# Performance work log

Measured on AMD Instinct MI355X. Metric: run time of the kernel, lower is better.

## Reference

```python
import jax, jax.numpy as jnp
import numpy as np


def setup_inputs() -> dict:
    B, S, DK, DV, H = 2, 2048, 1024, 1024, 16
    ks = jax.random.split(jax.random.key(0), 7)
    keys = jax.random.normal(ks[0], (B, S, DK), jnp.float32)
    queries = jax.random.normal(ks[1], (B, S, DK), jnp.float32)
    values = jax.random.normal(ks[2], (B, S, DV), jnp.float32)
    # per-head projection weights, stored as [H, in, out] (torch Linear uses W.T; math-equivalent)
    WQ = jax.random.normal(ks[3], (H, DK, DK // H), jnp.float32) / np.sqrt(DK).astype(np.float32)
    WK = jax.random.normal(ks[4], (H, DK, DK // H), jnp.float32) / np.sqrt(DK).astype(np.float32)
    WV = jax.random.normal(ks[5], (H, DV, DV // H), jnp.float32) / np.sqrt(DV).astype(np.float32)
    WO = jax.random.normal(ks[6], (DV, DV), jnp.float32) / np.sqrt(DV).astype(np.float32)
    return {"keys": keys, "queries": queries, "values": values,
            "WQ": WQ, "WK": WK, "WV": WV, "WO": WO, "masking": 1}


def reference(keys, queries, values, WQ, WK, WV, WO, masking):
    B, Sq, _ = queries.shape
    Sk = keys.shape[1]
    # batched per-head projections (original loops over heads in Python)
    Q = jnp.einsum('bqd,hde->bhqe', queries, WQ)   # [B,H,Sq,dh]
    K = jnp.einsum('bkd,hde->bhke', keys, WK)      # [B,H,Sk,dh]
    V = jnp.einsum('bkd,hde->bhke', values, WV)    # [B,H,Sk,dvh]
    q_idx = jnp.arange(Sq)[:, None]
    k_idx = jnp.arange(Sk)[None, :]
    causal = k_idx <= q_idx
    # NOTE: original never applies the slope m; bias = (i - j) for i<=j else 0, same for all heads
    bias = jnp.where(causal, (k_idx - q_idx).astype(jnp.float32), 0.0)
    scale = np.float32(1.0 / np.sqrt(Sk))  # original divides by sqrt(keys.shape[1])
    y = (jnp.einsum('bhqe,bhke->bhqk', Q, K) + bias) * scale
    if masking:
        y = jnp.where(causal, y, -jnp.inf)
    # original: F.softmax(y, 1) on [B,Sq,Sk] -> softmax over the QUERY axis
    z = jax.nn.softmax(y, axis=2)
    out = jnp.einsum('bhqk,bhke->bhqe', z, V)      # [B,H,Sq,dvh]
    out = out.transpose(0, 2, 1, 3).reshape(B, Sq, -1)  # concat heads on last dim
    return out @ WO
```

## Files before the change

### kernel.cpp

```cpp
#include <hip/hip_runtime.h>
#include <math.h>

#define SEQ    2048
#define DMODEL 1024
#define NH     16
#define DH     64
#define NB     2
#define BHN    (NB*NH)

static constexpr float SCALE  = 0.02209708691207961f;
static constexpr float SCALE2 = 0.02209708691207961f * 1.4426950408889634f;

typedef __attribute__((ext_vector_type(8))) short short8;
typedef __attribute__((ext_vector_type(4))) short short4v;
typedef __attribute__((ext_vector_type(4))) float f32x4;

__device__ __forceinline__ short f2bf(float f) {
    union { float f; unsigned u; } v; v.f = f;
    unsigned r = (v.u + 0x7FFFu + ((v.u >> 16) & 1u)) >> 16;
    return (short)r;
}

__device__ __forceinline__ unsigned pack_bf2(float a, float b) {
    union { float f; unsigned u; } ua, ub; ua.f = a; ub.f = b;
    return __builtin_amdgcn_perm(ub.u + 0x8000u, ua.u + 0x8000u, 0x07060302u);
}

__device__ __forceinline__ float bf2f(short s) {
    union { unsigned u; float f; } v; v.u = ((unsigned)(unsigned short)s) << 16;
    return v.f;
}

__device__ __forceinline__ float exp2_fast(float x) {
    float r;
    __asm__("v_exp_f32 %0, %1" : "=v"(r) : "v"(x));
    return r;
}

__device__ __forceinline__ void load16_lds(const short* g, short* l) {
    __builtin_amdgcn_global_load_lds(
        (const __attribute__((address_space(1))) unsigned int*)g,
        (__attribute__((address_space(3))) unsigned int*)l,
        16, 0, 0);
}

__device__ __forceinline__ void stage_rows(const short* g, short* s, int t, int ldg, int nIter) {
    int wave = t >> 6, lane = t & 63;
    #pragma unroll
    for (int i = 0; i < 4; ++i) {
        if (i >= nIter) break;
        int E   = i * 2048 + wave * 512 + lane * 8;
        int row = E >> 6;
        int blk = (lane & 7) ^ (row & 7);
        load16_lds(g + (size_t)row * ldg + blk * 8, s + i * 2048 + wave * 512);
    }
}

__device__ __forceinline__ short8 frag_sw(const short* s, int rowbase, int ks, int lane) {
    int m   = rowbase + (lane & 15);
    int q   = lane >> 4;
    int blk = (ks * 4 + q) ^ (m & 7);
    return *(const short8*)(s + m * 64 + blk * 8);
}

__global__ __launch_bounds__(256) void convert_all(
    const float* __restrict__ q, const float* __restrict__ k, const float* __restrict__ v,
    short* __restrict__ Xq, short* __restrict__ Xk, short* __restrict__ Xv,
    const float* __restrict__ WQ, const float* __restrict__ WK,
    const float* __restrict__ WV, const float* __restrict__ WO,
    short* __restrict__ WQt, short* __restrict__ WKt,
    short* __restrict__ WVt, short* __restrict__ WOt)
{
    __shared__ float Ts[64][68];
    const int lin = blockIdx.x;
    const int t = threadIdx.x;

    if (lin < 6144) {
        const int z = lin / 2048, bx = lin - z * 2048;
        const float* src = (z == 0) ? q : (z == 1) ? k : v;
        short* dst = (z == 0) ? Xq : (z == 1) ? Xk : Xv;
        size_t idx = ((size_t)bx * 256 + t) * 8;
        float4 a = *(const float4*)(src + idx);
        float4 b = *(const float4*)(src + idx + 4);
        short8 o;
        o[0] = f2bf(a.x); o[1] = f2bf(a.y); o[2] = f2bf(a.z); o[3] = f2bf(a.w);
        o[4] = f2bf(b.x); o[5] = f2bf(b.y); o[6] = f2bf(b.z); o[7] = f2bf(b.w);
        *(short8*)(dst + idx) = o;
        return;
    }

    const int wl = lin - 6144;
    const int z = wl >> 8, rem = wl & 255;
    const int k0 = (rem & 15) * 64;
    const int ny = rem >> 4;
    const float* W = (z == 0) ? WQ : (z == 1) ? WK : (z == 2) ? WV : WO;
    short* Wt = (z == 0) ? WQt : (z == 1) ? WKt : (z == 2) ? WVt : WOt;

    const int tr = t >> 4, tc4 = (t & 15) * 4;
    #pragma unroll
    for (int i = 0; i < 4; ++i) {
        int row = tr + i * 16;
        float4 v4;
        if (z < 3) v4 = *(const float4*)(W + (size_t)ny * DMODEL * DH + (size_t)(k0 + row) * DH + tc4);
        else       v4 = *(const float4*)(W + (size_t)(k0 + row) * DMODEL + ny * 64 + tc4);
        Ts[tc4 + 0][row] = v4.x; Ts[tc4 + 1][row] = v4.y;
        Ts[tc4 + 2][row] = v4.z; Ts[tc4 + 3][row] = v4.w;
    }
    __syncthreads();
    #pragma unroll
    for (int i = 0; i < 4; ++i) {
        int nl = tr + i * 16;
        short4v o;
        o[0] = f2bf(Ts[nl][tc4 + 0]); o[1] = f2bf(Ts[nl][tc4 + 1]);
        o[2] = f2bf(Ts[nl][tc4 + 2]); o[3] = f2bf(Ts[nl][tc4 + 3]);
        *(short4v*)(Wt + (size_t)(ny * 64 + nl) * DMODEL + k0 + tc4) = o;
    }
}

__global__ __launch_bounds__(256) void gemm_nt(
    const short* __restrict__ A0, const short* __restrict__ A1, const short* __restrict__ A2,
    const short* __restrict__ B0, const short* __restrict__ B1, const short* __restrict__ B2,
    short* __restrict__ Y0, short* __restrict__ Y1, short* __restrict__ Y2)
{
    const int z = blockIdx.z;
    const short* X  = (z == 0) ? A0 : (z == 1) ? A1 : A2;
    const short* Wt = (z == 0) ? B0 : (z == 1) ? B1 : B2;
    short* Y        = (z == 0) ? Y0 : (z == 1) ? Y1 : Y2;
    const bool vOrient = (z == 2);

    const int lin = blockIdx.y * 8 + blockIdx.x;
    const int n0 = (lin >> 5) * 128;
    const int m0 = (lin & 31) * 128;

    __shared__ short As[128 * 64];
    __shared__ short Bs[128 * 64];

    const int t = threadIdx.x;
    const int wave = t >> 6, lane = t & 63;
    const int wrow = (wave >> 1) * 64, wcol = (wave & 1) * 64;
    const int quad = lane >> 4, l15 = lane & 15;

    f32x4 acc[4][4];
    #pragma unroll
    for (int i = 0; i < 4; ++i)
        #pragma unroll
        for (int j = 0; j < 4; ++j)
            acc[i][j] = (f32x4)0.f;

    for (int k0 = 0; k0 < DMODEL; k0 += 64) {
        __syncthreads();
        stage_rows(X  + (size_t)m0 * DMODEL + k0, As, t, DMODEL, 4);
        stage_rows(Wt + (size_t)n0 * DMODEL + k0, Bs, t, DMODEL, 4);
        __syncthreads();
        if (!vOrient) {
            #pragma unroll
            for (int ks = 0; ks < 2; ++ks) {
                short8 xf[4], wf[4];
                #pragma unroll
                for (int i = 0; i < 4; ++i) xf[i] = frag_sw(As, wrow + i * 16, ks, lane);
                #pragma unroll
                for (int i = 0; i < 4; ++i) wf[i] = frag_sw(Bs, wcol + i * 16, ks, lane);
                #pragma unroll
                for (int a = 0; a < 4; ++a)
                    #pragma unroll
                    for (int b = 0; b < 4; ++b)
                        acc[a][b] = __builtin_amdgcn_mfma_f32_16x16x32_bf16(
                            wf[a], xf[b], acc[a][b], 0, 0, 0);
            }
        } else {
            #pragma unroll
            for (int ks = 0; ks < 2; ++ks) {
                short8 xf[4], wf[4];
                #pragma unroll
                for (int i = 0; i < 4; ++i) xf[i] = frag_sw(As, wrow + i * 16, ks, lane);
                #pragma unroll
                for (int i = 0; i < 4; ++i) wf[i] = frag_sw(Bs, wcol + i * 16, ks, lane);
                #pragma unroll
                for (int a = 0; a < 4; ++a)
                    #pragma unroll
                    for (int b = 0; b < 4; ++b)
                        acc[a][b] = __builtin_amdgcn_mfma_f32_16x16x32_bf16(
                            xf[a], wf[b], acc[a][b], 0, 0, 0);
            }
        }
    }

    if (vOrient) {
        #pragma unroll
        for (int a = 0; a < 4; ++a) {
            #pragma unroll
            for (int b = 0; b < 4; ++b) {
                int m = m0 + wrow + a * 16 + quad * 4;
                int n = n0 + wcol + b * 16 + l15;
                int bb = m >> 11, s = m & 2047, h = n >> 6, e = n & 63;
                short4v o;
                #pragma unroll
                for (int i = 0; i < 4; ++i) o[i] = f2bf(acc[a][b][i]);
                *(short4v*)(Y + ((size_t)((bb * NH + h) * DH + e)) * SEQ + s) = o;
            }
        }
    } else {
        #pragma unroll
        for (int a = 0; a < 4; ++a) {
            #pragma unroll
            for (int b = 0; b < 4; ++b) {
                int n = n0 + wcol + a * 16 + quad * 4;
                int m = m0 + wrow + b * 16 + l15;
                int bb = m >> 11, s = m & 2047, h = n >> 6, e = n & 63;
                short4v o;
                #pragma unroll
                for (int i = 0; i < 4; ++i) o[i] = f2bf(acc[a][b][i]);
                *(short4v*)(Y + ((size_t)((bb * NH + h) * SEQ + s)) * DH + e) = o;
            }
        }
    }
}

__global__ __launch_bounds__(256) void gemm_out(
    const short* __restrict__ X, const short* __restrict__ Wt,
    float* __restrict__ outF)
{
    const int lin = blockIdx.x;
    const int m0 = (lin & 31) * 128;
    const int n0 = (lin >> 5) * 64;

    __shared__ short As[2][128 * 64];
    __shared__ short Bs[2][64 * 64];

    const int t = threadIdx.x;
    const int wave = t >> 6, lane = t & 63;
    const int wrow = (wave >> 1) * 64, wcol = (wave & 1) * 32;
    const int quad = lane >> 4, l15 = lane & 15;

    f32x4 acc[2][4];
    #pragma unroll
    for (int i = 0; i < 2; ++i)
        #pragma unroll
        for (int j = 0; j < 4; ++j)
            acc[i][j] = (f32x4)0.f;

    stage_rows(X  + (size_t)m0 * DMODEL, As[0], t, DMODEL, 4);
    stage_rows(Wt + (size_t)n0 * DMODEL, Bs[0], t, DMODEL, 2);
    __syncthreads();

    int cur = 0;
    for (int it = 0; it < 16; ++it) {
        if (it + 1 < 16) {
            const int k0 = (it + 1) * 64;
            stage_rows(X  + (size_t)m0 * DMODEL + k0, As[cur ^ 1], t, DMODEL, 4);
            stage_rows(Wt + (size_t)n0 * DMODEL + k0, Bs[cur ^ 1], t, DMODEL, 2);
        }
        #pragma unroll
        for (int ks = 0; ks < 2; ++ks) {
            short8 xf[4], wf[2];
            #pragma unroll
            for (int i = 0; i < 4; ++i) xf[i] = frag_sw(As[cur], wrow + i * 16, ks, lane);
            #pragma unroll
            for (int i = 0; i < 2; ++i) wf[i] = frag_sw(Bs[cur], wcol + i * 16, ks, lane);
            #pragma unroll
            for (int a = 0; a < 2; ++a)
                #pragma unroll
                for (int b = 0; b < 4; ++b)
                    acc[a][b] = __builtin_amdgcn_mfma_f32_16x16x32_bf16(
                        wf[a], xf[b], acc[a][b], 0, 0, 0);
        }
        __syncthreads();
        cur ^= 1;
    }

    #pragma unroll
    for (int a = 0; a < 2; ++a) {
        #pragma unroll
        for (int b = 0; b < 4; ++b) {
            int n = n0 + wcol + a * 16 + quad * 4;
            int m = m0 + wrow + b * 16 + l15;
            float4 o = make_float4(acc[a][b][0], acc[a][b][1], acc[a][b][2], acc[a][b][3]);
            *(float4*)(outF + (size_t)m * DMODEL + n) = o;
        }
    }
}

__global__ __launch_bounds__(256) void stats_mfma(
    const short* __restrict__ Qg, const short* __restrict__ Kg,
    short* __restrict__ Vt, const int* __restrict__ mask_p)
{
    const int gblk = blockIdx.x;
    const int masking = mask_p[0];

    __shared__ short Ks[64 * 64];
    __shared__ short Qs[2][128 * 64];
    __shared__ float rsh[64];

    const int t = threadIdx.x;
    const int wave = t >> 6, lane = t & 63;
    const int quad = lane >> 4, l15 = lane & 15;

    for (int item = 0; item < 2; ++item) {
        const int w  = item ? (1023 - gblk) : gblk;
        const int kt = w >> 5, bh = w & 31;
        const int k0 = kt * 64;

        const int qb0 = masking ? (kt >> 1) : 0;
        const int q0s = qb0 * 128;
        if (item) __syncthreads();
        stage_rows(Kg + ((size_t)bh * SEQ + k0) * DH, Ks, t, DH, 2);
        stage_rows(Qg + ((size_t)bh * SEQ + q0s) * DH, Qs[0], t, DH, 4);
        __syncthreads();

        short8 Kf[2];
        Kf[0] = frag_sw(Ks, wave * 16, 0, lane);
        Kf[1] = frag_sw(Ks, wave * 16, 1, lane);

        int   kgi[4];
        float biasK[4];
        #pragma unroll
        for (int i = 0; i < 4; ++i) {
            kgi[i] = k0 + wave * 16 + quad * 4 + i;
            biasK[i] = SCALE2 * (float)kgi[i];
        }
        float qS[8];
        #pragma unroll
        for (int nt = 0; nt < 8; ++nt)
            qS[nt] = SCALE2 * (float)(q0s + nt * 16 + l15);

        float dsum[4] = {0.f, 0.f, 0.f, 0.f};
        const int nIter = masking ? (16 - qb0) : 16;
        for (int it = 0; it < nIter; ++it) {
            const int cur = it & 1;
            if (it > 0) __syncthreads();
            if (it + 1 < nIter)
                stage_rows(Qg + ((size_t)bh * SEQ + q0s + (it + 1) * 128) * DH, Qs[1 - cur], t, DH, 4);

            f32x4 acc[8];
            #pragma unroll
            for (int nt = 0; nt < 8; ++nt) acc[nt] = (f32x4)0.f;
            __builtin_amdgcn_s_setprio(1);
            #pragma unroll
            for (int ks = 0; ks < 2; ++ks)
                #pragma unroll
                for (int nt = 0; nt < 8; ++nt)
                    acc[nt] = __builtin_amdgcn_mfma_f32_16x16x32_bf16(
                        Kf[ks], frag_sw(Qs[cur], nt * 16, ks, lane), acc[nt], 0, 0, 0);
            __builtin_amdgcn_s_setprio(0);

            const bool exact = masking && (it == 0);
            #pragma unroll
            for (int nt = 0; nt < 8; ++nt) {
                #pragma unroll
                for (int i = 0; i < 4; ++i) {
                    float diff = biasK[i] - qS[nt];
                    float v = masking ? fmaf(acc[nt][i], SCALE2, diff)
                                      : fmaf(acc[nt][i], SCALE2, fminf(diff, 0.f));
                    float e = exp2_fast(v);
                    if (exact)
                        e = (kgi[i] <= (q0s + nt * 16 + l15)) ? e : 0.f;
                    dsum[i] += e;
                }
            }
            #pragma unroll
            for (int nt = 0; nt < 8; ++nt) qS[nt] += 128.f * SCALE2;
        }

        #pragma unroll
        for (int i = 0; i < 4; ++i) {
            float d = dsum[i];
            #pragma unroll
            for (int mm = 1; mm < 16; mm <<= 1) d += __shfl_xor(d, mm);
            dsum[i] = d;
        }
        if (l15 == 0) {
            #pragma unroll
            for (int i = 0; i < 4; ++i)
                rsh[wave * 16 + quad * 4 + i] = 1.f / dsum[i];
        }
        __syncthreads();

        short* Vs = Vt + (size_t)bh * DH * SEQ + k0;
        const int e  = t >> 2;
        const int sc = (t & 3) * 16;
        short8 v0 = *(short8*)(Vs + (size_t)e * SEQ + sc);
        short8 v1 = *(short8*)(Vs + (size_t)e * SEQ + sc + 8);
        union { unsigned u[4]; short8 s8; } o0, o1;
        #pragma unroll
        for (int j = 0; j < 4; ++j) {
            o0.u[j] = pack_bf2(bf2f(v0[2 * j])     * rsh[sc + 2 * j],
                               bf2f(v0[2 * j + 1]) * rsh[sc + 2 * j + 1]);
            o1.u[j] = pack_bf2(bf2f(v1[2 * j])     * rsh[sc + 8 + 2 * j],
                               bf2f(v1[2 * j + 1]) * rsh[sc + 8 + 2 * j + 1]);
        }
        *(short8*)(Vs + (size_t)e * SEQ + sc)     = o0.s8;
        *(short8*)(Vs + (size_t)e * SEQ + sc + 8) = o1.s8;
    }
}

template<int MODE>
__device__ __forceinline__ void attn_tile(
    const short* Kbuf, const short* Vbuf, short* Pw,
    const short8 Qf[2], const float bias[4][4], f32x4 oacc[4],
    int lane, int quad, int l15, int qloc)
{
    f32x4 sacc[4];
    #pragma unroll
    for (int mt = 0; mt < 4; ++mt) sacc[mt] = (f32x4)0.f;
    __builtin_amdgcn_s_setprio(1);
    #pragma unroll
    for (int ks = 0; ks < 2; ++ks) {
        #pragma unroll
        for (int mt = 0; mt < 4; ++mt)
            sacc[mt] = __builtin_amdgcn_mfma_f32_16x16x32_bf16(
                frag_sw(Kbuf, mt * 16, ks, lane), Qf[ks], sacc[mt], 0, 0, 0);
    }
    __builtin_amdgcn_s_setprio(0);
    __asm__ volatile("" ::: "memory");
    #pragma unroll
    for (int mt = 0; mt < 4; ++mt) {
        float p[4];
        #pragma unroll
        for (int i = 0; i < 4; ++i) {
            float bi = bias[mt][i];
            float v = (MODE == 2) ? fmaf(sacc[mt][i], SCALE2, fminf(bi, 0.f))
                                  : fmaf(sacc[mt][i], SCALE2, bi);
            float e = exp2_fast(v);
            if (MODE == 1)
                e = ((mt * 16 + quad * 4 + i) <= qloc) ? e : 0.f;
            p[i] = e;
        }
        int blk = (2 * mt + (quad >> 1)) ^ (l15 & 7);
        *(uint2*)(Pw + l15 * 64 + blk * 8 + (quad & 1) * 4) =
            make_uint2(pack_bf2(p[0], p[1]), pack_bf2(p[2], p[3]));
    }
    __asm__ volatile("" ::: "memory");
    __builtin_amdgcn_s_setprio(1);
    #pragma unroll
    for (int ks = 0; ks < 2; ++ks) {
        short8 pf = *(const short8*)(Pw + l15 * 64 + (((ks * 4 + quad) ^ (l15 & 7)) * 8));
        #pragma unroll
        for (int mt = 0; mt < 4; ++mt)
            oacc[mt] = __builtin_amdgcn_mfma_f32_16x16x32_bf16(
                frag_sw(Vbuf, mt * 16, ks, lane), pf, oacc[mt], 0, 0, 0);
    }
    __builtin_amdgcn_s_setprio(0);
}

__global__ __launch_bounds__(256) void attn_mfma(
    const short* __restrict__ Qg, const short* __restrict__ Kg, const short* __restrict__ Vt,
    short* __restrict__ attnb, const int* __restrict__ mask_p)
{
    const int gblk = blockIdx.x;
    const int masking = mask_p[0];

    __shared__ short Qs[64 * 64];
    __shared__ short Ks[2][64 * 64];
    __shared__ short Vts[2][64 * 64];

    const int t = threadIdx.x;
    const int wave = t >> 6, lane = t & 63;
    const int quad = lane >> 4, l15 = lane & 15;
    short* Pw = Qs + wave * 1024;
    const int qloc = wave * 16 + l15;

    for (int item = 0; item < 2; ++item) {
        const int w  = item ? (1023 - gblk) : gblk;
        const int qt = w >> 5, bh = w & 31;
        const int b = bh >> 4, h = bh & (NH - 1);
        const int q0 = qt * 64;

        if (item) __syncthreads();
        stage_rows(Qg + ((size_t)bh * SEQ + q0) * DH, Qs, t, DH, 2);
        stage_rows(Kg + (size_t)bh * SEQ * DH, Ks[0], t, DH, 2);
        stage_rows(Vt + (size_t)bh * DH * SEQ, Vts[0], t, SEQ, 2);
        __syncthreads();

        short8 Qf[2];
        Qf[0] = frag_sw(Qs, wave * 16, 0, lane);
        Qf[1] = frag_sw(Qs, wave * 16, 1, lane);

        float bias[4][4];
        #pragma unroll
        for (int mt = 0; mt < 4; ++mt)
            #pragma unroll
            for (int i = 0; i < 4; ++i)
                bias[mt][i] = SCALE2 * (float)((mt * 16 + quad * 4 + i)
                                             - (q0 + qloc));

        f32x4 oacc[4];
        #pragma unroll
        for (int mt = 0; mt < 4; ++mt) oacc[mt] = (f32x4)0.f;

        const int nIter = masking ? (qt + 1) : (SEQ / 64);
        for (int it = 0; it < nIter; ++it) {
            const int cur = it & 1;
            if (it > 0) __syncthreads();
            if (it + 1 < nIter) {
                const int k0n = (it + 1) * 64;
                stage_rows(Kg + ((size_t)bh * SEQ + k0n) * DH, Ks[1 - cur], t, DH, 2);
                stage_rows(Vt + (size_t)bh * DH * SEQ + k0n, Vts[1 - cur], t, SEQ, 2);
            }
            if (!masking)       attn_tile<2>(Ks[cur], Vts[cur], Pw, Qf, bias, oacc, lane, quad, l15, qloc);
            else if (it == qt)  attn_tile<1>(Ks[cur], Vts[cur], Pw, Qf, bias, oacc, lane, quad, l15, qloc);
            else                attn_tile<0>(Ks[cur], Vts[cur], Pw, Qf, bias, oacc, lane, quad, l15, qloc);
            #pragma unroll
            for (int mt = 0; mt < 4; ++mt)
                #pragma unroll
                for (int i = 0; i < 4; ++i)
                    bias[mt][i] += 64.f * SCALE2;
        }

        #pragma unroll
        for (int mt = 0; mt < 4; ++mt) {
            int e = mt * 16 + quad * 4;
            int q = q0 + wave * 16 + l15;
            short4v o;
            #pragma unroll
            for (int i = 0; i < 4; ++i) o[i] = f2bf(oacc[mt][i]);
            *(short4v*)(attnb + ((size_t)(b * SEQ + q)) * DMODEL + h * DH + e) = o;
        }
    }
}

extern "C" void kernel_launch(void* const* d_in, const int* in_sizes, int n_in,
                              void* d_out, int out_size, void* d_ws, size_t ws_size,
                              hipStream_t stream) {
    const float* keys    = (const float*)d_in[0];
    const float* queries = (const float*)d_in[1];
    const float* values  = (const float*)d_in[2];
    const float* WQ      = (const float*)d_in[3];
    const float* WK      = (const float*)d_in[4];
    const float* WV      = (const float*)d_in[5];
    const float* WO      = (const float*)d_in[6];
    const int*   mask_p  = (const int*)d_in[7];
    float* out = (float*)d_out;

    const size_t nX = (size_t)NB * SEQ * DMODEL;
    const size_t nW = (size_t)DMODEL * DMODEL;
    const size_t nQ = (size_t)BHN * SEQ * DH;

    short* ws = (short*)d_ws;
    short* Xq    = ws;
    short* Xk    = Xq + nX;
    short* Xv    = Xk + nX;
    short* WQt   = Xv + nX;
    short* WKt   = WQt + nW;
    short* WVt   = WKt + nW;
    short* WOt   = WVt + nW;
    short* Qg    = WOt + nW;
    short* Kg    = Qg + nQ;
    short* Vtg   = Kg + nQ;
    short* attnb = Vtg + nQ;

    convert_all<<<dim3(7168), dim3(256), 0, stream>>>(
        queries, keys, values, Xq, Xk, Xv,
        WQ, WK, WV, WO, WQt, WKt, WVt, WOt);
    gemm_nt<<<dim3(8, 32, 3), dim3(256), 0, stream>>>(
        Xq, Xk, Xv, WQt, WKt, WVt, Qg, Kg, Vtg);
    stats_mfma<<<dim3(512), dim3(256), 0, stream>>>(Qg, Kg, Vtg, mask_p);
    attn_mfma<<<dim3(512), dim3(256), 0, stream>>>(Qg, Kg, Vtg, attnb, mask_p);
    gemm_out<<<dim3(512), dim3(256), 0, stream>>>(attnb, WOt, out);
}
```

Before: 239.3 us.

## Double-buffer QKV projection GEMM and shrink N tile to 64

Rewrites the QKV projection GEMM to use double-buffered shared memory, so the next K-slice is loaded while MFMAs run on the current one, with one barrier per iteration. The block tile shrinks from 128x128 to 128x64, which doubles the grid to 512 blocks per matrix and halves the accumulators per wave. This aims to hide global-load latency and raise occupancy and wave count across the CUs. In exchange, weight-tile reuse per block drops and A tiles are loaded twice as often.

```diff
diff --git a/kernel.cpp b/kernel.cpp
--- a/kernel.cpp
+++ b/kernel.cpp
@@ -128,80 +128,85 @@
     short* Y        = (z == 0) ? Y0 : (z == 1) ? Y1 : Y2;
     const bool vOrient = (z == 2);
 
-    const int lin = blockIdx.y * 8 + blockIdx.x;
-    const int n0 = (lin >> 5) * 128;
+    const int lin = blockIdx.x;
     const int m0 = (lin & 31) * 128;
-
-    __shared__ short As[128 * 64];
-    __shared__ short Bs[128 * 64];
+    const int n0 = (lin >> 5) * 64;
+
+    __shared__ short As[2][128 * 64];
+    __shared__ short Bs[2][64 * 64];
 
     const int t = threadIdx.x;
     const int wave = t >> 6, lane = t & 63;
-    const int wrow = (wave >> 1) * 64, wcol = (wave & 1) * 64;
+    const int wrow = (wave >> 1) * 64, wcol = (wave & 1) * 32;
     const int quad = lane >> 4, l15 = lane & 15;
 
-    f32x4 acc[4][4];
-    #pragma unroll
-    for (int i = 0; i < 4; ++i)
-        #pragma unroll
-        for (int j = 0; j < 4; ++j)
-            acc[i][j] = (f32x4)0.f;
-
-    for (int k0 = 0; k0 < DMODEL; k0 += 64) {
-        __syncthreads();
-        stage_rows(X  + (size_t)m0 * DMODEL + k0, As, t, DMODEL, 4);
-        stage_rows(Wt + (size_t)n0 * DMODEL + k0, Bs, t, DMODEL, 4);
-        __syncthreads();
+    f32x4 acc[8];
+    #pragma unroll
+    for (int i = 0; i < 8; ++i) acc[i] = (f32x4)0.f;
+
+    stage_rows(X  + (size_t)m0 * DMODEL, As[0], t, DMODEL, 4);
+    stage_rows(Wt + (size_t)n0 * DMODEL, Bs[0], t, DMODEL, 2);
+    __syncthreads();
+
+    int cur = 0;
+    for (int it = 0; it < 16; ++it) {
+        if (it + 1 < 16) {
+            const int k0 = (it + 1) * 64;
+            stage_rows(X  + (size_t)m0 * DMODEL + k0, As[cur ^ 1], t, DMODEL, 4);
+            stage_rows(Wt + (size_t)n0 * DMODEL + k0, Bs[cur ^ 1], t, DMODEL, 2);
+        }
         if (!vOrient) {
             #pragma unroll
             for (int ks = 0; ks < 2; ++ks) {
-                short8 xf[4], wf[4];
-                #pragma unroll
-                for (int i = 0; i < 4; ++i) xf[i] = frag_sw(As, wrow + i * 16, ks, lane);
-                #pragma unroll
-                for (int i = 0; i < 4; ++i) wf[i] = frag_sw(Bs, wcol + i * 16, ks, lane);
+                short8 xf[4], wf[2];
+                #pragma unroll
+                for (int i = 0; i < 4; ++i) xf[i] = frag_sw(As[cur], wrow + i * 16, ks, lane);
+                #pragma unroll
+                for (int i = 0; i < 2; ++i) wf[i] = frag_sw(Bs[cur], wcol + i * 16, ks, lane);
+                #pragma unroll
+                for (int a = 0; a < 2; ++a)
+                    #pragma unroll
+                    for (int b = 0; b < 4; ++b)
+                        acc[a * 4 + b] = __builtin_amdgcn_mfma_f32_16x16x32_bf16(
+                            wf[a], xf[b], acc[a * 4 + b], 0, 0, 0);
+            }
+        } else {
+            #pragma unroll
+            for (int ks = 0; ks < 2; ++ks) {
+                short8 xf[4], wf[2];
+                #pragma unroll
+                for (int i = 0; i < 4; ++i) xf[i] = frag_sw(As[cur], wrow + i * 16, ks, lane);
+                #pragma unroll
+                for (int i = 0; i < 2; ++i) wf[i] = frag_sw(Bs[cur], wcol + i * 16, ks, lane);
                 #pragma unroll
                 for (int a = 0; a < 4; ++a)
                     #pragma unroll
-                    for (int b = 0; b < 4; ++b)
-                        acc[a][b] = __builtin_amdgcn_mfma_f32_16x16x32_bf16(
-                            wf[a], xf[b], acc[a][b], 0, 0, 0);
+                    for (int b = 0; b < 2; ++b)
+                        acc[a * 2 + b] = __builtin_amdgcn_mfma_f32_16x16x32_bf16(
+                            xf[a], wf[b], acc[a * 2 + b], 0, 0, 0);
             }
-        } else {
-            #pragma unroll
-            for (int ks = 0; ks < 2; ++ks) {
-                short8 xf[4], wf[4];
-                #pragma unroll
-                for (int i = 0; i < 4; ++i) xf[i] = frag_sw(As, wrow + i * 16, ks, lane);
-                #pragma unroll
-                for (int i = 0; i < 4; ++i) wf[i] = frag_sw(Bs, wcol + i * 16, ks, lane);
-                #pragma unroll
-                for (int a = 0; a < 4; ++a)
-                    #pragma unroll
-                    for (int b = 0; b < 4; ++b)
-                        acc[a][b] = __builtin_amdgcn_mfma_f32_16x16x32_bf16(
-                            xf[a], wf[b], acc[a][b], 0, 0, 0);
-            }
-        }
+        }
+        __syncthreads();
+        cur ^= 1;
     }
 
     if (vOrient) {
         #pragma unroll
         for (int a = 0; a < 4; ++a) {
             #pragma unroll
-            for (int b = 0; b < 4; ++b) {
+            for (int b = 0; b < 2; ++b) {
                 int m = m0 + wrow + a * 16 + quad * 4;
                 int n = n0 + wcol + b * 16 + l15;
                 int bb = m >> 11, s = m & 2047, h = n >> 6, e = n & 63;
                 short4v o;
                 #pragma unroll
-                for (int i = 0; i < 4; ++i) o[i] = f2bf(acc[a][b][i]);
+                for (int i = 0; i < 4; ++i) o[i] = f2bf(acc[a * 2 + b][i]);
                 *(short4v*)(Y + ((size_t)((bb * NH + h) * DH + e)) * SEQ + s) = o;
             }
         }
     } else {
         #pragma unroll
-        for (int a = 0; a < 4; ++a) {
+        for (int a = 0; a < 2; ++a) {
             #pragma unroll
             for (int b = 0; b < 4; ++b) {
                 int n = n0 + wcol + a * 16 + quad * 4;
@@ -209,7 +214,7 @@
                 int bb = m >> 11, s = m & 2047, h = n >> 6, e = n & 63;
                 short4v o;
                 #pragma unroll
-                for (int i = 0; i < 4; ++i) o[i] = f2bf(acc[a][b][i]);
+                for (int i = 0; i < 4; ++i) o[i] = f2bf(acc[a * 4 + b][i]);
                 *(short4v*)(Y + ((size_t)((bb * NH + h) * SEQ + s)) * DH + e) = o;
             }
         }
@@ -551,7 +556,7 @@
     convert_all<<<dim3(7168), dim3(256), 0, stream>>>(
         queries, keys, values, Xq, Xk, Xv,
         WQ, WK, WV, WO, WQt, WKt, WVt, WOt);
-    gemm_nt<<<dim3(8, 32, 3), dim3(256), 0, stream>>>(
+    gemm_nt<<<dim3(512, 1, 3), dim3(256), 0, stream>>>(
         Xq, Xk, Xv, WQt, WKt, WVt, Qg, Kg, Vtg);
     stats_mfma<<<dim3(512), dim3(256), 0, stream>>>(Qg, Kg, Vtg, mask_p);
     attn_mfma<<<dim3(512), dim3(256), 0, stream>>>(Qg, Kg, Vtg, attnb, mask_p);
```

Result: faster. 231.5 us (-3.3%).
